# Performance work log

Hardware: AMD Instinct MI355X
Metric: run time of the kernel (lower is better)

Reference implementation:

```python
import jax, jax.numpy as jnp
import numpy as np

NUM_HEADS = 4   # num_heads init kwarg
KERNEL = 7      # kernel_size init kwarg
EPS = 1e-5      # nn.LayerNorm default eps


def setup_inputs() -> dict:
    key = jax.random.key(0)
    ks = jax.random.split(key, 6)
    C, depth = 128, 2
    x = jax.random.normal(ks[0], (2, C, 64, 64), jnp.float32)
    qkv_w = jax.random.normal(ks[1], (depth, 3 * C, C), jnp.float32) * 0.05
    qkv_b = jnp.zeros((depth, 3 * C), jnp.float32)
    rpb = jax.random.normal(ks[2], (depth, NUM_HEADS, 2 * KERNEL - 1, 2 * KERNEL - 1), jnp.float32) * 0.02
    proj_w = jax.random.normal(ks[3], (depth, C, C), jnp.float32) * 0.05
    proj_b = jnp.zeros((depth, C), jnp.float32)
    ln_g = jnp.ones((C,), jnp.float32)
    ln_b = jnp.zeros((C,), jnp.float32)
    return dict(x=x, qkv_w=qkv_w, qkv_b=qkv_b, rpb=rpb,
                proj_w=proj_w, proj_b=proj_b, ln_g=ln_g, ln_b=ln_b)


def _na2d(x, w_qkv, b_qkv, rpb, w_p, b_p):
    """NATTEN-style 2D neighborhood attention. x: (B,H,W,C)."""
    B, H, W, C = x.shape
    h, k = NUM_HEADS, KERNEL
    d = C // h
    qkv = (x @ w_qkv.T + b_qkv).reshape(B, H, W, 3, h, d)
    q = qkv[..., 0, :, :] * (d ** -0.5)   # (B,H,W,h,d)
    kk = qkv[..., 1, :, :]
    v = qkv[..., 2, :, :]
    # edge-clamped window starts: each query sees exactly k x k neighbors
    si = jnp.clip(jnp.arange(H) - k // 2, 0, H - k)
    sj = jnp.clip(jnp.arange(W) - k // 2, 0, W - k)
    idx_i = si[:, None] + jnp.arange(k)   # (H,k) absolute row indices
    idx_j = sj[:, None] + jnp.arange(k)   # (W,k) absolute col indices

    def win(t):  # (B,H,W,h,d) -> (B,H,W,k,k,h,d)
        t = t[:, idx_i]          # (B,H,k,W,h,d)
        t = t[:, :, :, idx_j]    # (B,H,k,W,k,h,d)
        return jnp.transpose(t, (0, 1, 3, 2, 4, 5, 6))

    kw = win(kk)
    vw = win(v)
    attn = jnp.einsum('bijhd,bijpqhd->bijhpq', q, kw)  # (B,H,W,h,k,k)
    # relative position bias: index = (neighbor_abs - query) + (k-1)
    bi = jnp.arange(k)[None, :] + (k - 1) - (jnp.arange(H) - si)[:, None]  # (H,k)
    bj = jnp.arange(k)[None, :] + (k - 1) - (jnp.arange(W) - sj)[:, None]  # (W,k)
    bias = rpb[:, bi[:, None, :, None], bj[None, :, None, :]]  # (h,H,W,k,k)
    attn = attn + jnp.transpose(bias, (1, 2, 0, 3, 4))[None]
    attn = jax.nn.softmax(attn.reshape(B, H, W, h, k * k), axis=-1).reshape(B, H, W, h, k, k)
    out = jnp.einsum('bijhpq,bijpqhd->bijhd', attn, vw).reshape(B, H, W, C)
    return out @ w_p.T + b_p


def reference(x, qkv_w, qkv_b, rpb, proj_w, proj_b, ln_g, ln_b):
    y = jnp.transpose(x, (0, 2, 3, 1))  # NCHW -> NHWC
    for l in range(qkv_w.shape[0]):     # depth=2 stacked NA layers
        y = _na2d(y, qkv_w[l], qkv_b[l], rpb[l], proj_w[l], proj_b[l])
    mu = y.mean(-1, keepdims=True)
    var = y.var(-1, keepdims=True)
    y = (y - mu) / jnp.sqrt(var + EPS) * ln_g + ln_b
    return jnp.transpose(y, (0, 3, 1, 2))  # NHWC -> NCHW
```

## Files before the change

kernel.cpp:

```cpp
#include <hip/hip_runtime.h>
#include <hip/hip_bf16.h>
#include <math.h>

#define PIX 8192
typedef __hip_bfloat16 bf16;
typedef __attribute__((ext_vector_type(8))) short short8;
typedef __attribute__((ext_vector_type(4))) float f32x4;

__device__ inline float bflo(unsigned u) { return __uint_as_float(u << 16); }
__device__ inline float bfhi(unsigned u) { return __uint_as_float(u & 0xffff0000u); }
__device__ inline unsigned short f2b(float f) {
  __hip_bfloat16 h = __float2bfloat16(f);
  return *reinterpret_cast<unsigned short*>(&h);
}
__device__ inline unsigned pack2(float a, float b) {
  return (unsigned)f2b(a) | ((unsigned)f2b(b) << 16);
}
__device__ inline short8 ldw8(const float* __restrict__ p) {
  f32x4 lo = *(const f32x4*)p;
  f32x4 hi = *(const f32x4*)(p + 4);
  short8 r;
  r[0] = (short)f2b(lo[0]); r[1] = (short)f2b(lo[1]);
  r[2] = (short)f2b(lo[2]); r[3] = (short)f2b(lo[3]);
  r[4] = (short)f2b(hi[0]); r[5] = (short)f2b(hi[1]);
  r[6] = (short)f2b(hi[2]); r[7] = (short)f2b(hi[3]);
  return r;
}

__global__ __launch_bounds__(256) void xqkv_cvt(const float* __restrict__ x,
                                                const float* __restrict__ qw,
                                                const float* __restrict__ qb,
                                                unsigned short* __restrict__ qkv,
                                                const float* __restrict__ pw,
                                                unsigned short* __restrict__ wq1,
                                                unsigned short* __restrict__ wp) {
  if (blockIdx.x >= 512) {
    int idx = (blockIdx.x - 512) * 256 + threadIdx.x;
    wq1[idx] = f2b(qw[49152 + idx]);
    wq1[idx + 16384] = f2b(qw[49152 + idx + 16384]);
    if (idx < 16384) wq1[idx + 32768] = f2b(qw[49152 + idx + 32768]);
    wp[idx] = f2b(pw[idx]);
    return;
  }

  __shared__ __align__(16) unsigned short As[16 * 136];
  int m0 = blockIdx.x * 16;
  int tid = threadIdx.x;
  int b = m0 >> 12, i = (m0 >> 6) & 63, j0 = m0 & 63;

  for (int idx = tid; idx < 2048; idx += 256) {
    int c = idx >> 4, jl = idx & 15;
    As[jl * 136 + c] =
        f2b(x[(size_t)b * 524288 + (size_t)c * 4096 + i * 64 + j0 + jl]);
  }
  __syncthreads();

  int w = tid >> 6, lane = tid & 63;
  int quad = lane >> 4, l16 = lane & 15;
  short8 a[4];
#pragma unroll
  for (int kc = 0; kc < 4; ++kc)
    a[kc] = *(const short8*)(As + l16 * 136 + kc * 32 + quad * 8);
#pragma unroll
  for (int nt = 0; nt < 6; ++nt) {
    int col = w * 96 + nt * 16 + l16;
    const float* wrow = qw + (size_t)col * 128 + quad * 8;
    f32x4 c = {0.f, 0.f, 0.f, 0.f};
#pragma unroll
    for (int kc = 0; kc < 4; ++kc)
      c = __builtin_amdgcn_mfma_f32_16x16x32_bf16(a[kc], ldw8(wrow + kc * 32), c, 0, 0, 0);
    float bv = qb[col];
#pragma unroll
    for (int r2 = 0; r2 < 4; ++r2)
      qkv[(size_t)(m0 + quad * 4 + r2) * 384 + col] = f2b(c[r2] + bv);
  }
}

__global__ __launch_bounds__(256) void gemm_mfma(const unsigned short* __restrict__ A,
                                                 const unsigned short* __restrict__ W,
                                                 const float* __restrict__ bias,
                                                 unsigned short* __restrict__ Cmat,
                                                 int N) {
  int m0 = blockIdx.x * 64, n0 = blockIdx.y * 64;
  int tid = threadIdx.x;
  int w = tid >> 6, lane = tid & 63;
  int quad = lane >> 4, l16 = lane & 15;

  const short8* ap =
      (const short8*)(A + (size_t)(m0 + w * 16 + l16) * 128 + quad * 8);
  short8 a[4];
#pragma unroll
  for (int kc = 0; kc < 4; ++kc) a[kc] = ap[kc * 4];

  f32x4 acc[4];
#pragma unroll
  for (int nt = 0; nt < 4; ++nt) {
    const short8* bp =
        (const short8*)(W + (size_t)(n0 + nt * 16 + l16) * 128 + quad * 8);
    f32x4 c = {0.f, 0.f, 0.f, 0.f};
#pragma unroll
    for (int kc = 0; kc < 4; ++kc)
      c = __builtin_amdgcn_mfma_f32_16x16x32_bf16(a[kc], bp[kc * 4], c, 0, 0, 0);
    acc[nt] = c;
  }

#pragma unroll
  for (int nt = 0; nt < 4; ++nt) {
    int col = n0 + nt * 16 + l16;
    float bv = bias[col];
#pragma unroll
    for (int r = 0; r < 4; ++r) {
      int m = m0 + w * 16 + quad * 4 + r;
      Cmat[(size_t)m * N + col] = f2b(acc[nt][r] + bv);
    }
  }
}

#define RSTRIDE 136
__global__ __launch_bounds__(512, 1) void attnproj(const unsigned short* __restrict__ qkvp,
                                                   const float* __restrict__ rpb,
                                                   const unsigned short* __restrict__ wp,
                                                   const float* __restrict__ pbias,
                                                   unsigned short* __restrict__ y) {
  __shared__ __align__(16) unsigned short kbuf[140 * RSTRIDE];
  __shared__ __align__(16) unsigned short vbuf[140 * RSTRIDE];
  __shared__ float rb[676];
  __shared__ float sc[128][52];

  int ti = blockIdx.x >> 4, tj = blockIdx.x & 15;
  int bz = blockIdx.y;
  int tid = threadIdx.x;
  int bi0 = ti * 8 - 3, bj0 = tj * 4 - 3;

  for (int t = tid; t < 676; t += 512) rb[t] = rpb[t];

  for (int t = tid; t < 4480; t += 512) {
    int row = t >> 5;
    int sub = t & 31;
    int isv = sub >> 4;
    int c = sub & 15;
    int ri = row / 10, rj = row - ri * 10;
    int gi = bi0 + ri, gj = bj0 + rj;
    uint4 val = make_uint4(0, 0, 0, 0);
    if ((unsigned)gi < 64u && (unsigned)gj < 64u) {
      int pixn = (bz * 64 + gi) * 64 + gj;
      val = *(const uint4*)(qkvp + (size_t)pixn * 384 + 128 + isv * 128 + c * 8);
    }
    *(uint4*)((isv ? vbuf : kbuf) + row * RSTRIDE + c * 8) = val;
  }
  __syncthreads();

  int r = tid & 3;
  int hh = (tid >> 2) & 3;
  int px = tid >> 4;
  int ph = px * 4 + hh;
  int pi = px >> 2, pj = px & 3;
  int i = ti * 8 + pi, j = tj * 4 + pj;
  int si = min(max(i - 3, 0), 57), sj = min(max(j - 3, 0), 57);
  int li = si - bi0, lj = sj - bj0;
  int oi = i - si, oj = j - sj;
  int pix = (bz * 64 + i) * 64 + j;

  const float scale = 0.17677669529663687f;
  float q[8];
  {
    uint4 t = *(const uint4*)(qkvp + (size_t)pix * 384 + hh * 32 + r * 8);
    q[0] = bflo(t.x) * scale;  q[1] = bfhi(t.x) * scale;
    q[2] = bflo(t.y) * scale;  q[3] = bfhi(t.y) * scale;
    q[4] = bflo(t.z) * scale;  q[5] = bfhi(t.z) * scale;
    q[6] = bflo(t.w) * scale;  q[7] = bfhi(t.w) * scale;
  }

  const unsigned short* kh = kbuf + hh * 32 + r * 8;
  const unsigned short* vh = vbuf + hh * 32 + r * 8;
  const float* rbh = rb + hh * 169;

#pragma unroll
  for (int p = 0; p < 7; ++p) {
#pragma unroll
    for (int qq = 0; qq < 7; ++qq) {
      int n = (li + p) * 10 + (lj + qq);
      uint4 t = *(const uint4*)(kh + n * RSTRIDE);
      float dot = q[0] * bflo(t.x) + q[1] * bfhi(t.x)
                + q[2] * bflo(t.y) + q[3] * bfhi(t.y)
                + q[4] * bflo(t.z) + q[5] * bfhi(t.z)
                + q[6] * bflo(t.w) + q[7] * bfhi(t.w);
      dot += __shfl_xor(dot, 1);
      dot += __shfl_xor(dot, 2);
      if (r == 0) sc[ph][p * 7 + qq] = dot + rbh[(p + 6 - oi) * 13 + (qq + 6 - oj)];
    }
  }
  __syncthreads();

  float m = -INFINITY;
#pragma unroll
  for (int n = 0; n < 49; ++n) m = fmaxf(m, sc[ph][n]);

  float sum = 0.f;
  float acc[8] = {0.f, 0.f, 0.f, 0.f, 0.f, 0.f, 0.f, 0.f};
#pragma unroll
  for (int p = 0; p < 7; ++p) {
#pragma unroll
    for (int qq = 0; qq < 7; ++qq) {
      float e = __expf(sc[ph][p * 7 + qq] - m);
      sum += e;
      int n = (li + p) * 10 + (lj + qq);
      uint4 t = *(const uint4*)(vh + n * RSTRIDE);
      acc[0] += e * bflo(t.x);  acc[1] += e * bfhi(t.x);
      acc[2] += e * bflo(t.y);  acc[3] += e * bfhi(t.y);
      acc[4] += e * bflo(t.z);  acc[5] += e * bfhi(t.z);
      acc[6] += e * bflo(t.w);  acc[7] += e * bfhi(t.w);
    }
  }
  float inv = 1.f / sum;
  uint4 t;
  t.x = pack2(acc[0] * inv, acc[1] * inv);
  t.y = pack2(acc[2] * inv, acc[3] * inv);
  t.z = pack2(acc[4] * inv, acc[5] * inv);
  t.w = pack2(acc[6] * inv, acc[7] * inv);
  unsigned short* obuf = kbuf;
  *(uint4*)(obuf + px * RSTRIDE + hh * 32 + r * 8) = t;
  __syncthreads();

  int w = tid >> 6, lane = tid & 63;
  int quad = lane >> 4, l16 = lane & 15;
  int mt = w & 1;
  int ng = w >> 1;
  short8 a[4];
#pragma unroll
  for (int kc = 0; kc < 4; ++kc)
    a[kc] = *(const short8*)(obuf + (mt * 16 + l16) * RSTRIDE + kc * 32 + quad * 8);
#pragma unroll
  for (int s = 0; s < 2; ++s) {
    int col = (ng * 2 + s) * 16 + l16;
    const short8* bp = (const short8*)(wp + (size_t)col * 128 + quad * 8);
    f32x4 c = {0.f, 0.f, 0.f, 0.f};
#pragma unroll
    for (int kc = 0; kc < 4; ++kc)
      c = __builtin_amdgcn_mfma_f32_16x16x32_bf16(a[kc], bp[kc * 4], c, 0, 0, 0);
    float bv = pbias[col];
#pragma unroll
    for (int r2 = 0; r2 < 4; ++r2) {
      int mloc = mt * 16 + quad * 4 + r2;
      int gpix = (bz * 64 + ti * 8 + (mloc >> 2)) * 64 + tj * 4 + (mloc & 3);
      y[(size_t)gpix * 128 + col] = f2b(c[r2] + bv);
    }
  }
}

__global__ __launch_bounds__(256) void ln_out(const unsigned short* __restrict__ y,
                                              const float* __restrict__ g,
                                              const float* __restrict__ bta,
                                              float* __restrict__ out) {
  __shared__ float tile[64][129];
  __shared__ float mean_s[64], rstd_s[64];
  int blk = blockIdx.x;
  int b = blk >> 6, i = blk & 63;
  int tid = threadIdx.x;
  const unsigned short* yrow = y + (size_t)blk * 64 * 128;
  int jj = tid >> 2, qtr = tid & 3;
  float sum = 0.f, sumsq = 0.f;
#pragma unroll
  for (int u = 0; u < 4; ++u) {
    int c = qtr * 32 + u * 8;
    uint4 t = *(const uint4*)(yrow + jj * 128 + c);
    float v0 = bflo(t.x), v1 = bfhi(t.x), v2 = bflo(t.y), v3 = bfhi(t.y);
    float v4 = bflo(t.z), v5 = bfhi(t.z), v6 = bflo(t.w), v7 = bfhi(t.w);
    sum += v0 + v1 + v2 + v3 + v4 + v5 + v6 + v7;
    sumsq += v0*v0 + v1*v1 + v2*v2 + v3*v3 + v4*v4 + v5*v5 + v6*v6 + v7*v7;
    tile[jj][c+0] = v0; tile[jj][c+1] = v1; tile[jj][c+2] = v2; tile[jj][c+3] = v3;
    tile[jj][c+4] = v4; tile[jj][c+5] = v5; tile[jj][c+6] = v6; tile[jj][c+7] = v7;
  }
  sum += __shfl_xor(sum, 1);  sum += __shfl_xor(sum, 2);
  sumsq += __shfl_xor(sumsq, 1);  sumsq += __shfl_xor(sumsq, 2);
  if (qtr == 0) {
    float mu = sum * (1.f / 128.f);
    mean_s[jj] = mu;
    rstd_s[jj] = rsqrtf(sumsq * (1.f / 128.f) - mu * mu + 1e-5f);
  }
  __syncthreads();
  int c0 = tid >> 6;
  int j = tid & 63;
  for (int c = c0; c < 128; c += 4) {
    float v = (tile[j][c] - mean_s[j]) * rstd_s[j] * g[c] + bta[c];
    out[(((size_t)b * 128 + c) * 64 + i) * 64 + j] = v;
  }
}

extern "C" void kernel_launch(void* const* d_in, const int* in_sizes, int n_in,
                              void* d_out, int out_size, void* d_ws, size_t ws_size,
                              hipStream_t stream) {
  (void)in_sizes; (void)n_in; (void)out_size; (void)ws_size;
  const float* x   = (const float*)d_in[0];
  const float* qw  = (const float*)d_in[1];
  const float* qb  = (const float*)d_in[2];
  const float* rpb = (const float*)d_in[3];
  const float* pw  = (const float*)d_in[4];
  const float* pb  = (const float*)d_in[5];
  const float* lg  = (const float*)d_in[6];
  const float* lb  = (const float*)d_in[7];

  unsigned short* y    = (unsigned short*)d_ws;
  unsigned short* qkv  = y + (size_t)PIX * 128;
  unsigned short* wq1  = qkv + (size_t)PIX * 384;
  unsigned short* wp   = wq1 + 49152;
  float* out = (float*)d_out;

  xqkv_cvt<<<640, 256, 0, stream>>>(x, qw, qb, qkv, pw, wq1, wp);
  attnproj<<<dim3(128, 2), 512, 0, stream>>>(qkv, rpb, wp, pb, y);
  gemm_mfma<<<dim3(128, 6), 256, 0, stream>>>(y, wq1, qb + 384, qkv, 384);
  attnproj<<<dim3(128, 2), 512, 0, stream>>>(qkv, rpb + 676, wp + 16384, pb + 128, y);
  ln_out<<<128, 256, 0, stream>>>(y, lg, lb, out);
}
```

Before: 139.1 us.

## Fuse next-layer QKV GEMM and final LayerNorm into attention-projection kernel

The attention+projection kernel now keeps its projected output tile in shared memory and, depending on a template mode, either runs the next layer's QKV GEMM directly into a second qkv buffer, or applies the final LayerNorm and writes NCHW output. This removes two kernel launches and the global round trip of the intermediate y tensor. It uses a separate ping-pong qkv buffer since other blocks still read the first one's halo, and adds extra per-block MFMA work and weight loads to a kernel that launches only 256 blocks.

```diff
diff --git a/kernel.cpp b/kernel.cpp
--- a/kernel.cpp
+++ b/kernel.cpp
@@ -76,52 +76,18 @@
   }
 }
 
-__global__ __launch_bounds__(256) void gemm_mfma(const unsigned short* __restrict__ A,
-                                                 const unsigned short* __restrict__ W,
-                                                 const float* __restrict__ bias,
-                                                 unsigned short* __restrict__ Cmat,
-                                                 int N) {
-  int m0 = blockIdx.x * 64, n0 = blockIdx.y * 64;
-  int tid = threadIdx.x;
-  int w = tid >> 6, lane = tid & 63;
-  int quad = lane >> 4, l16 = lane & 15;
-
-  const short8* ap =
-      (const short8*)(A + (size_t)(m0 + w * 16 + l16) * 128 + quad * 8);
-  short8 a[4];
-#pragma unroll
-  for (int kc = 0; kc < 4; ++kc) a[kc] = ap[kc * 4];
-
-  f32x4 acc[4];
-#pragma unroll
-  for (int nt = 0; nt < 4; ++nt) {
-    const short8* bp =
-        (const short8*)(W + (size_t)(n0 + nt * 16 + l16) * 128 + quad * 8);
-    f32x4 c = {0.f, 0.f, 0.f, 0.f};
-#pragma unroll
-    for (int kc = 0; kc < 4; ++kc)
-      c = __builtin_amdgcn_mfma_f32_16x16x32_bf16(a[kc], bp[kc * 4], c, 0, 0, 0);
-    acc[nt] = c;
-  }
-
-#pragma unroll
-  for (int nt = 0; nt < 4; ++nt) {
-    int col = n0 + nt * 16 + l16;
-    float bv = bias[col];
-#pragma unroll
-    for (int r = 0; r < 4; ++r) {
-      int m = m0 + w * 16 + quad * 4 + r;
-      Cmat[(size_t)m * N + col] = f2b(acc[nt][r] + bv);
-    }
-  }
-}
-
 #define RSTRIDE 136
+template <int MODE>
 __global__ __launch_bounds__(512, 1) void attnproj(const unsigned short* __restrict__ qkvp,
                                                    const float* __restrict__ rpb,
                                                    const unsigned short* __restrict__ wp,
                                                    const float* __restrict__ pbias,
-                                                   unsigned short* __restrict__ y) {
+                                                   const unsigned short* __restrict__ wq1,
+                                                   const float* __restrict__ qb1,
+                                                   unsigned short* __restrict__ qkvo,
+                                                   const float* __restrict__ g,
+                                                   const float* __restrict__ bta,
+                                                   float* __restrict__ out) {
   __shared__ __align__(16) unsigned short kbuf[140 * RSTRIDE];
   __shared__ __align__(16) unsigned short vbuf[140 * RSTRIDE];
   __shared__ float rb[676];
@@ -222,68 +188,84 @@
   *(uint4*)(obuf + px * RSTRIDE + hh * 32 + r * 8) = t;
   __syncthreads();
 
+  unsigned short* ybuf = vbuf;
   int w = tid >> 6, lane = tid & 63;
   int quad = lane >> 4, l16 = lane & 15;
   int mt = w & 1;
   int ng = w >> 1;
-  short8 a[4];
-#pragma unroll
-  for (int kc = 0; kc < 4; ++kc)
-    a[kc] = *(const short8*)(obuf + (mt * 16 + l16) * RSTRIDE + kc * 32 + quad * 8);
-#pragma unroll
-  for (int s = 0; s < 2; ++s) {
-    int col = (ng * 2 + s) * 16 + l16;
-    const short8* bp = (const short8*)(wp + (size_t)col * 128 + quad * 8);
-    f32x4 c = {0.f, 0.f, 0.f, 0.f};
+  {
+    short8 a[4];
 #pragma unroll
     for (int kc = 0; kc < 4; ++kc)
-      c = __builtin_amdgcn_mfma_f32_16x16x32_bf16(a[kc], bp[kc * 4], c, 0, 0, 0);
-    float bv = pbias[col];
-#pragma unroll
-    for (int r2 = 0; r2 < 4; ++r2) {
-      int mloc = mt * 16 + quad * 4 + r2;
-      int gpix = (bz * 64 + ti * 8 + (mloc >> 2)) * 64 + tj * 4 + (mloc & 3);
-      y[(size_t)gpix * 128 + col] = f2b(c[r2] + bv);
-    }
-  }
-}
-
-__global__ __launch_bounds__(256) void ln_out(const unsigned short* __restrict__ y,
-                                              const float* __restrict__ g,
-                                              const float* __restrict__ bta,
-                                              float* __restrict__ out) {
-  __shared__ float tile[64][129];
-  __shared__ float mean_s[64], rstd_s[64];
-  int blk = blockIdx.x;
-  int b = blk >> 6, i = blk & 63;
-  int tid = threadIdx.x;
-  const unsigned short* yrow = y + (size_t)blk * 64 * 128;
-  int jj = tid >> 2, qtr = tid & 3;
-  float sum = 0.f, sumsq = 0.f;
-#pragma unroll
-  for (int u = 0; u < 4; ++u) {
-    int c = qtr * 32 + u * 8;
-    uint4 t = *(const uint4*)(yrow + jj * 128 + c);
-    float v0 = bflo(t.x), v1 = bfhi(t.x), v2 = bflo(t.y), v3 = bfhi(t.y);
-    float v4 = bflo(t.z), v5 = bfhi(t.z), v6 = bflo(t.w), v7 = bfhi(t.w);
-    sum += v0 + v1 + v2 + v3 + v4 + v5 + v6 + v7;
-    sumsq += v0*v0 + v1*v1 + v2*v2 + v3*v3 + v4*v4 + v5*v5 + v6*v6 + v7*v7;
-    tile[jj][c+0] = v0; tile[jj][c+1] = v1; tile[jj][c+2] = v2; tile[jj][c+3] = v3;
-    tile[jj][c+4] = v4; tile[jj][c+5] = v5; tile[jj][c+6] = v6; tile[jj][c+7] = v7;
-  }
-  sum += __shfl_xor(sum, 1);  sum += __shfl_xor(sum, 2);
-  sumsq += __shfl_xor(sumsq, 1);  sumsq += __shfl_xor(sumsq, 2);
-  if (qtr == 0) {
-    float mu = sum * (1.f / 128.f);
-    mean_s[jj] = mu;
-    rstd_s[jj] = rsqrtf(sumsq * (1.f / 128.f) - mu * mu + 1e-5f);
-  }
-  __syncthreads();
-  int c0 = tid >> 6;
-  int j = tid & 63;
-  for (int c = c0; c < 128; c += 4) {
-    float v = (tile[j][c] - mean_s[j]) * rstd_s[j] * g[c] + bta[c];
-    out[(((size_t)b * 128 + c) * 64 + i) * 64 + j] = v;
+      a[kc] = *(const short8*)(obuf + (mt * 16 + l16) * RSTRIDE + kc * 32 + quad * 8);
+#pragma unroll
+    for (int s = 0; s < 2; ++s) {
+      int col = (ng * 2 + s) * 16 + l16;
+      const short8* bp = (const short8*)(wp + (size_t)col * 128 + quad * 8);
+      f32x4 c = {0.f, 0.f, 0.f, 0.f};
+#pragma unroll
+      for (int kc = 0; kc < 4; ++kc)
+        c = __builtin_amdgcn_mfma_f32_16x16x32_bf16(a[kc], bp[kc * 4], c, 0, 0, 0);
+      float bv = pbias[col];
+#pragma unroll
+      for (int r2 = 0; r2 < 4; ++r2)
+        ybuf[(mt * 16 + quad * 4 + r2) * RSTRIDE + col] = f2b(c[r2] + bv);
+    }
+  }
+  __syncthreads();
+
+  if constexpr (MODE == 0) {
+    short8 ay[2][4];
+#pragma unroll
+    for (int mt2 = 0; mt2 < 2; ++mt2)
+#pragma unroll
+      for (int kc = 0; kc < 4; ++kc)
+        ay[mt2][kc] = *(const short8*)(ybuf + (mt2 * 16 + l16) * RSTRIDE + kc * 32 + quad * 8);
+#pragma unroll
+    for (int s = 0; s < 3; ++s) {
+      int col = (w * 3 + s) * 16 + l16;
+      const short8* bp = (const short8*)(wq1 + (size_t)col * 128 + quad * 8);
+      float bv = qb1[col];
+#pragma unroll
+      for (int mt2 = 0; mt2 < 2; ++mt2) {
+        f32x4 c = {0.f, 0.f, 0.f, 0.f};
+#pragma unroll
+        for (int kc = 0; kc < 4; ++kc)
+          c = __builtin_amdgcn_mfma_f32_16x16x32_bf16(ay[mt2][kc], bp[kc * 4], c, 0, 0, 0);
+#pragma unroll
+        for (int r2 = 0; r2 < 4; ++r2) {
+          int mloc = mt2 * 16 + quad * 4 + r2;
+          int gpix = (bz * 64 + ti * 8 + (mloc >> 2)) * 64 + tj * 4 + (mloc & 3);
+          qkvo[(size_t)gpix * 384 + col] = f2b(c[r2] + bv);
+        }
+      }
+    }
+  } else {
+    int px2 = tid >> 4, sub = tid & 15;
+    uint4 tv = *(const uint4*)(ybuf + px2 * RSTRIDE + sub * 8);
+    float v[8];
+    v[0] = bflo(tv.x); v[1] = bfhi(tv.x); v[2] = bflo(tv.y); v[3] = bfhi(tv.y);
+    v[4] = bflo(tv.z); v[5] = bfhi(tv.z); v[6] = bflo(tv.w); v[7] = bfhi(tv.w);
+    float sum2 = 0.f, sumsq = 0.f;
+#pragma unroll
+    for (int k = 0; k < 8; ++k) { sum2 += v[k]; sumsq += v[k] * v[k]; }
+    sum2 += __shfl_xor(sum2, 1);  sumsq += __shfl_xor(sumsq, 1);
+    sum2 += __shfl_xor(sum2, 2);  sumsq += __shfl_xor(sumsq, 2);
+    sum2 += __shfl_xor(sum2, 4);  sumsq += __shfl_xor(sumsq, 4);
+    sum2 += __shfl_xor(sum2, 8);  sumsq += __shfl_xor(sumsq, 8);
+    float mu = sum2 * (1.f / 128.f);
+    float rstd = rsqrtf(sumsq * (1.f / 128.f) - mu * mu + 1e-5f);
+    int i2 = ti * 8 + (px2 >> 2), j2 = tj * 4 + (px2 & 3);
+    int c0 = sub * 8;
+    f32x4 g0 = *(const f32x4*)(g + c0),   g1 = *(const f32x4*)(g + c0 + 4);
+    f32x4 b0 = *(const f32x4*)(bta + c0), b1 = *(const f32x4*)(bta + c0 + 4);
+#pragma unroll
+    for (int k = 0; k < 8; ++k) {
+      float gg = (k < 4) ? g0[k] : g1[k - 4];
+      float bb = (k < 4) ? b0[k] : b1[k - 4];
+      float o = (v[k] - mu) * rstd * gg + bb;
+      out[(((size_t)bz * 128 + c0 + k) * 64 + i2) * 64 + j2] = o;
+    }
   }
 }
 
@@ -300,15 +282,17 @@
   const float* lg  = (const float*)d_in[6];
   const float* lb  = (const float*)d_in[7];
 
-  unsigned short* y    = (unsigned short*)d_ws;
-  unsigned short* qkv  = y + (size_t)PIX * 128;
-  unsigned short* wq1  = qkv + (size_t)PIX * 384;
+  unsigned short* qkvA = (unsigned short*)d_ws;
+  unsigned short* qkvB = qkvA + (size_t)PIX * 384;
+  unsigned short* wq1  = qkvB + (size_t)PIX * 384;
   unsigned short* wp   = wq1 + 49152;
   float* out = (float*)d_out;
 
-  xqkv_cvt<<<640, 256, 0, stream>>>(x, qw, qb, qkv, pw, wq1, wp);
-  attnproj<<<dim3(128, 2), 512, 0, stream>>>(qkv, rpb, wp, pb, y);
-  gemm_mfma<<<dim3(128, 6), 256, 0, stream>>>(y, wq1, qb + 384, qkv, 384);
-  attnproj<<<dim3(128, 2), 512, 0, stream>>>(qkv, rpb + 676, wp + 16384, pb + 128, y);
-  ln_out<<<128, 256, 0, stream>>>(y, lg, lb, out);
-}
+  xqkv_cvt<<<640, 256, 0, stream>>>(x, qw, qb, qkvA, pw, wq1, wp);
+  attnproj<0><<<dim3(128, 2), 512, 0, stream>>>(qkvA, rpb, wp, pb, wq1,
+                                                qb + 384, qkvB, nullptr,
+                                                nullptr, nullptr);
+  attnproj<1><<<dim3(128, 2), 512, 0, stream>>>(qkvB, rpb + 676, wp + 16384,
+                                                pb + 128, nullptr, nullptr,
+                                                nullptr, lg, lb, out);
+}
```

After: 130.4 us. -6.2%, faster.
